# Kernel tuning notes

Hardware: AMD Instinct MI355X
Metric: run time of the kernel (lower is better)

The kernel has to match this reference:

```python
import jax, jax.numpy as jnp
import numpy as np

SIGMA = 1.0

def setup_inputs() -> dict:
    key = jax.random.key(0)
    kx, ky = jax.random.split(key)
    x = jax.random.normal(kx, (8192, 256), dtype=jnp.float32)
    y = jax.random.normal(ky, (8192, 256), dtype=jnp.float32)
    return {"x": x, "y": y}

def reference(x, y):
    x2 = jnp.sum(x * x, axis=-1)            # [N]
    y2 = jnp.sum(y * y, axis=-1)            # [M]
    d2 = x2[:, None] + y2[None, :] - 2.0 * (x @ y.T)  # [N, M]
    d2 = jnp.maximum(d2, 0.0)
    k = jnp.exp(-d2 / (2.0 * SIGMA ** 2))
    # original: exp(...)[None].sum(dim=0).mean() == mean over all N*M entries
    return jnp.mean(k)
```

## Files before the change

kernel.cpp:

```cpp
#include <hip/hip_runtime.h>
#include <hip/hip_fp8.h>

#define NROWS 8192
#define DIM   256

typedef float f32x4 __attribute__((ext_vector_type(4)));
typedef long  i64x2 __attribute__((ext_vector_type(2)));

typedef __attribute__((address_space(3))) char lds_char;
typedef __attribute__((address_space(1))) const char glob_char;

#define LOG2E  1.4426950408889634f
#define NEG_HALF_LOG2E (-0.7213475204444817f)

__device__ __forceinline__ int pack4_fp8(float a, float b, float c, float d) {
#if __has_builtin(__builtin_amdgcn_cvt_pk_fp8_f32)
    int pk = __builtin_amdgcn_cvt_pk_fp8_f32(a, b, 0, false);
    pk     = __builtin_amdgcn_cvt_pk_fp8_f32(c, d, pk, true);
    return pk;
#else
    union { unsigned char by[4]; int i; } u;
    u.by[0] = __hip_fp8_e4m3(a).__x;
    u.by[1] = __hip_fp8_e4m3(b).__x;
    u.by[2] = __hip_fp8_e4m3(c).__x;
    u.by[3] = __hip_fp8_e4m3(d).__x;
    return u.i;
#endif
}

__global__ __launch_bounds__(256) void prep_kernel(
    const float* __restrict__ x, const float* __restrict__ y,
    unsigned char* __restrict__ xb, unsigned char* __restrict__ yb,
    float* __restrict__ px, float* __restrict__ py,
    float* __restrict__ out)
{
    int tid  = threadIdx.x;
    int lane = tid & 63;
    int w    = tid >> 6;
    int row  = blockIdx.x * 4 + w;
    bool isx = row < NROWS;
    int r    = isx ? row : row - NROWS;
    const float* src = (isx ? x : y) + (size_t)r * DIM;
    float4 v = reinterpret_cast<const float4*>(src)[lane];
    float sq = v.x*v.x + v.y*v.y + v.z*v.z + v.w*v.w;
    #pragma unroll
    for (int off = 32; off; off >>= 1) sq += __shfl_xor(sq, off);

    int pk = pack4_fp8(v.x, v.y, v.z, v.w);
    int k0 = lane * 4;
    int kt = k0 >> 6, q = k0 & 63;
    int s  = q >> 5, hh = (q >> 3) & 3, j0 = q & 7;
    int p0 = (kt << 6) + (hh << 4) + (s << 3) + j0;
    unsigned char* dst = (isx ? xb : yb) + (size_t)r * DIM + p0;
    *reinterpret_cast<int*>(dst) = pk;

    if (lane == 0) (isx ? px : py)[r] = NEG_HALF_LOG2E * sq;
    if (blockIdx.x == 0 && tid == 0) out[0] = 0.0f;
}

__global__ __launch_bounds__(512, 6) void rbf_gemm_kernel(
    const unsigned char* __restrict__ xb, const unsigned char* __restrict__ yb,
    const float* __restrict__ px, const float* __restrict__ py,
    float* __restrict__ out)
{
    __shared__ __align__(16) char smem[33824];
    float* pxl = (float*)(smem + 32768);
    float* pyl = (float*)(smem + 33280);
    float* red = (float*)(smem + 33792);

    int tid  = threadIdx.x;
    int lane = tid & 63;
    int wv   = tid >> 6;
    int wm   = wv >> 2;
    int wn   = wv & 3;
    int b    = blockIdx.x;
    int c    = b & 7;
    int s    = b >> 3;
    int bm   = ((s >> 6) << 3) | c;
    int bn   = s & 63;
    int h    = lane >> 4;
    int l15  = lane & 15;

    f32x4 acc[4][2];
    #pragma unroll
    for (int m = 0; m < 4; ++m)
        #pragma unroll
        for (int n = 0; n < 2; ++n)
            acc[m][n] = (f32x4){0.f, 0.f, 0.f, 0.f};

    auto stage = [&](int buf, int kt) {
        char* base = smem + buf * 16384;
        int hh = tid >> 7, row = tid & 127;
        __builtin_amdgcn_global_load_lds(
            (glob_char*)((const char*)xb + (size_t)(bm * 128 + row) * 256 + kt * 64 + hh * 16),
            (lds_char*)(base + tid * 16), 16, 0, 0);
        __builtin_amdgcn_global_load_lds(
            (glob_char*)((const char*)yb + (size_t)(bn * 128 + row) * 256 + kt * 64 + hh * 16),
            (lds_char*)(base + 8192 + tid * 16), 16, 0, 0);
    };

    auto compute = [&](int buf) {
        const char* Ab = smem + buf * 16384;
        const char* Bb = Ab + 8192;
        i64x2 aF[4], bF[2];
        #pragma unroll
        for (int mf = 0; mf < 4; ++mf)
            aF[mf] = *reinterpret_cast<const i64x2*>(
                Ab + h * 2048 + (wm * 64 + mf * 16 + l15) * 16);
        #pragma unroll
        for (int nf = 0; nf < 2; ++nf)
            bF[nf] = *reinterpret_cast<const i64x2*>(
                Bb + h * 2048 + (wn * 32 + nf * 16 + l15) * 16);
        #pragma unroll
        for (int mf = 0; mf < 4; ++mf)
            #pragma unroll
            for (int nf = 0; nf < 2; ++nf) {
                acc[mf][nf] = __builtin_amdgcn_mfma_f32_16x16x32_fp8_fp8(
                    aF[mf][0], bF[nf][0], acc[mf][nf], 0, 0, 0);
                acc[mf][nf] = __builtin_amdgcn_mfma_f32_16x16x32_fp8_fp8(
                    aF[mf][1], bF[nf][1], acc[mf][nf], 0, 0, 0);
            }
    };

    if (tid < 128) {
        __builtin_amdgcn_global_load_lds(
            (glob_char*)((const char*)(px + bm * 128) + tid * 4),
            (lds_char*)((char*)pxl + tid * 4), 4, 0, 0);
        __builtin_amdgcn_global_load_lds(
            (glob_char*)((const char*)(py + bn * 128) + tid * 4),
            (lds_char*)((char*)pyl + tid * 4), 4, 0, 0);
    }
    stage(0, 0);
    __syncthreads();

    stage(1, 1); compute(0); __syncthreads();
    stage(0, 2); compute(1); __syncthreads();
    stage(1, 3); compute(0); __syncthreads();
    compute(1);

    float lsum = 0.f;
    float py2[2];
    #pragma unroll
    for (int nf = 0; nf < 2; ++nf) py2[nf] = pyl[wn * 32 + nf * 16 + l15];
    #pragma unroll
    for (int mf = 0; mf < 4; ++mf) {
        f32x4 pxv = *reinterpret_cast<const f32x4*>(pxl + wm * 64 + mf * 16 + h * 4);
        #pragma unroll
        for (int r = 0; r < 4; ++r) {
            float pv = pxv[r];
            #pragma unroll
            for (int nf = 0; nf < 2; ++nf)
                lsum += exp2f(fmaf(acc[mf][nf][r], LOG2E, pv + py2[nf]));
        }
    }
    #pragma unroll
    for (int off = 32; off; off >>= 1) lsum += __shfl_xor(lsum, off);
    if (lane == 0) red[wv] = lsum;
    __syncthreads();
    if (tid == 0) {
        float ss = (red[0] + red[1] + red[2] + red[3] +
                    red[4] + red[5] + red[6] + red[7]) * 1.4901161193847656e-08f;
        atomicAdd(out, ss);
    }
}

extern "C" void kernel_launch(void* const* d_in, const int* in_sizes, int n_in,
                              void* d_out, int out_size, void* d_ws, size_t ws_size,
                              hipStream_t stream) {
    const float* x = (const float*)d_in[0];
    const float* y = (const float*)d_in[1];
    float* out = (float*)d_out;
    char* ws = (char*)d_ws;
    unsigned char* xb = (unsigned char*)ws;
    unsigned char* yb = (unsigned char*)(ws + (size_t)2 * 1024 * 1024);
    float* px = (float*)(ws + (size_t)4 * 1024 * 1024);
    float* py = (float*)(ws + (size_t)4 * 1024 * 1024 + 32 * 1024);

    hipLaunchKernelGGL(prep_kernel, dim3(4096), dim3(256), 0, stream,
                       x, y, xb, yb, px, py, out);
    hipLaunchKernelGGL(rbf_gemm_kernel, dim3(4096), dim3(512), 0, stream,
                       xb, yb, px, py, out);
}
```

Measured before the change: 130.2 us.

## Switch to scaled 16x16x128 FP8 MFMA with K=128 tiles and new data layout

Replaces the pair of 16x16x32 FP8 MFMAs per fragment with a single MFMA-scale 16x16x128 f8f6f4 instruction using unit E8M0 scales, halving the K iterations to two stages of 128. The prep kernel reorders fp8 bytes into a new K-interleaved layout to match the wider fragment, LDS tiles double to 64KB, and occupancy hint drops from 6 to 4 blocks. It also changes block-to-tile swizzle. This aims to cut MFMA issue count and loop/sync overhead at the cost of more LDS per block and lower occupancy.

```diff
diff --git a/kernel.cpp b/kernel.cpp
--- a/kernel.cpp
+++ b/kernel.cpp
@@ -5,13 +5,15 @@
 #define DIM   256
 
 typedef float f32x4 __attribute__((ext_vector_type(4)));
-typedef long  i64x2 __attribute__((ext_vector_type(2)));
+typedef int   i32x4 __attribute__((ext_vector_type(4)));
+typedef int   i32x8 __attribute__((ext_vector_type(8)));
 
 typedef __attribute__((address_space(3))) char lds_char;
 typedef __attribute__((address_space(1))) const char glob_char;
 
 #define LOG2E  1.4426950408889634f
 #define NEG_HALF_LOG2E (-0.7213475204444817f)
+#define UNIT_SCALE 0x7F7F7F7F
 
 __device__ __forceinline__ int pack4_fp8(float a, float b, float c, float d) {
 #if __has_builtin(__builtin_amdgcn_cvt_pk_fp8_f32)
@@ -48,9 +50,11 @@
 
     int pk = pack4_fp8(v.x, v.y, v.z, v.w);
     int k0 = lane * 4;
-    int kt = k0 >> 6, q = k0 & 63;
-    int s  = q >> 5, hh = (q >> 3) & 3, j0 = q & 7;
-    int p0 = (kt << 6) + (hh << 4) + (s << 3) + j0;
+    int kt = k0 >> 7;
+    int h  = (k0 >> 5) & 3;
+    int j2 = (k0 >> 4) & 1;
+    int b0 = k0 & 15;
+    int p0 = kt * 128 + j2 * 64 + h * 16 + b0;
     unsigned char* dst = (isx ? xb : yb) + (size_t)r * DIM + p0;
     *reinterpret_cast<int*>(dst) = pk;
 
@@ -58,15 +62,15 @@
     if (blockIdx.x == 0 && tid == 0) out[0] = 0.0f;
 }
 
-__global__ __launch_bounds__(512, 6) void rbf_gemm_kernel(
+__global__ __launch_bounds__(512, 4) void rbf_gemm_kernel(
     const unsigned char* __restrict__ xb, const unsigned char* __restrict__ yb,
     const float* __restrict__ px, const float* __restrict__ py,
     float* __restrict__ out)
 {
-    __shared__ __align__(16) char smem[33824];
-    float* pxl = (float*)(smem + 32768);
-    float* pyl = (float*)(smem + 33280);
-    float* red = (float*)(smem + 33792);
+    __shared__ __align__(16) char smem[66592];
+    float* pxl = (float*)(smem + 65536);
+    float* pyl = (float*)(smem + 66048);
+    float* red = (float*)(smem + 66560);
 
     int tid  = threadIdx.x;
     int lane = tid & 63;
@@ -74,10 +78,8 @@
     int wm   = wv >> 2;
     int wn   = wv & 3;
     int b    = blockIdx.x;
-    int c    = b & 7;
-    int s    = b >> 3;
-    int bm   = ((s >> 6) << 3) | c;
-    int bn   = s & 63;
+    int bm   = (b & 7) * 8 + (b >> 9);
+    int bn   = (b >> 3) & 63;
     int h    = lane >> 4;
     int l15  = lane & 15;
 
@@ -89,37 +91,47 @@
             acc[m][n] = (f32x4){0.f, 0.f, 0.f, 0.f};
 
     auto stage = [&](int buf, int kt) {
-        char* base = smem + buf * 16384;
-        int hh = tid >> 7, row = tid & 127;
-        __builtin_amdgcn_global_load_lds(
-            (glob_char*)((const char*)xb + (size_t)(bm * 128 + row) * 256 + kt * 64 + hh * 16),
-            (lds_char*)(base + tid * 16), 16, 0, 0);
-        __builtin_amdgcn_global_load_lds(
-            (glob_char*)((const char*)yb + (size_t)(bn * 128 + row) * 256 + kt * 64 + hh * 16),
-            (lds_char*)(base + 8192 + tid * 16), 16, 0, 0);
+        char* base = smem + buf * 32768;
+        #pragma unroll
+        for (int j = 0; j < 2; ++j) {
+            int e = j * 512 + tid;
+            int j2h = e >> 7, row = e & 127;
+            __builtin_amdgcn_global_load_lds(
+                (glob_char*)((const char*)xb + (size_t)(bm * 128 + row) * 256 + kt * 128 + j2h * 16),
+                (lds_char*)(base + e * 16), 16, 0, 0);
+            __builtin_amdgcn_global_load_lds(
+                (glob_char*)((const char*)yb + (size_t)(bn * 128 + row) * 256 + kt * 128 + j2h * 16),
+                (lds_char*)(base + 16384 + e * 16), 16, 0, 0);
+        }
     };
 
     auto compute = [&](int buf) {
-        const char* Ab = smem + buf * 16384;
-        const char* Bb = Ab + 8192;
-        i64x2 aF[4], bF[2];
+        const char* Ab = smem + buf * 32768;
+        const char* Bb = Ab + 16384;
+        i32x8 aF[4], bF[2];
         #pragma unroll
-        for (int mf = 0; mf < 4; ++mf)
-            aF[mf] = *reinterpret_cast<const i64x2*>(
-                Ab + h * 2048 + (wm * 64 + mf * 16 + l15) * 16);
+        for (int mf = 0; mf < 4; ++mf) {
+            int row = wm * 64 + mf * 16 + l15;
+            i32x4 r0 = *reinterpret_cast<const i32x4*>(Ab + (0 + h) * 2048 + row * 16);
+            i32x4 r1 = *reinterpret_cast<const i32x4*>(Ab + (4 + h) * 2048 + row * 16);
+            aF[mf] = __builtin_shufflevector(r0, r1, 0, 1, 2, 3, 4, 5, 6, 7);
+        }
         #pragma unroll
-        for (int nf = 0; nf < 2; ++nf)
-            bF[nf] = *reinterpret_cast<const i64x2*>(
-                Bb + h * 2048 + (wn * 32 + nf * 16 + l15) * 16);
+        for (int nf = 0; nf < 2; ++nf) {
+            int row = wn * 32 + nf * 16 + l15;
+            i32x4 r0 = *reinterpret_cast<const i32x4*>(Bb + (0 + h) * 2048 + row * 16);
+            i32x4 r1 = *reinterpret_cast<const i32x4*>(Bb + (4 + h) * 2048 + row * 16);
+            bF[nf] = __builtin_shufflevector(r0, r1, 0, 1, 2, 3, 4, 5, 6, 7);
+        }
         #pragma unroll
         for (int mf = 0; mf < 4; ++mf)
             #pragma unroll
-            for (int nf = 0; nf < 2; ++nf) {
-                acc[mf][nf] = __builtin_amdgcn_mfma_f32_16x16x32_fp8_fp8(
-                    aF[mf][0], bF[nf][0], acc[mf][nf], 0, 0, 0);
-                acc[mf][nf] = __builtin_amdgcn_mfma_f32_16x16x32_fp8_fp8(
-                    aF[mf][1], bF[nf][1], acc[mf][nf], 0, 0, 0);
-            }
+            for (int nf = 0; nf < 2; ++nf)
+                acc[mf][nf] = __builtin_amdgcn_mfma_scale_f32_16x16x128_f8f6f4(
+                    aF[mf], bF[nf], acc[mf][nf],
+                    0, 0,
+                    0, UNIT_SCALE,
+                    0, UNIT_SCALE);
     };
 
     if (tid < 128) {
@@ -133,9 +145,9 @@
     stage(0, 0);
     __syncthreads();
 
-    stage(1, 1); compute(0); __syncthreads();
-    stage(0, 2); compute(1); __syncthreads();
-    stage(1, 3); compute(0); __syncthreads();
+    stage(1, 1);
+    compute(0);
+    __syncthreads();
     compute(1);
 
     float lsum = 0.f;
```

New measurement: 127.3 us. 1.02x faster.
